# Optimization experiments

Measured on AMD Instinct MI355X. Metric: run time of the kernel, lower is better.

Reference implementation:

```python
import jax, jax.numpy as jnp
import numpy as np

N_NODES = 100000
D_IN = 256
D_OUT = 128
N_EDGES = 1600000


def setup_inputs() -> dict:
    key = jax.random.key(0)
    k1, k2, k3, k4 = jax.random.split(key, 4)
    x = jax.random.normal(k1, (N_NODES, D_IN), dtype=jnp.float32)
    edge_index = jax.random.randint(k2, (2, N_EDGES), 0, N_NODES, dtype=jnp.int64)
    # GCNConv parameters (glorot-style scale)
    W = jax.random.normal(k3, (D_IN, D_OUT), dtype=jnp.float32) * (1.0 / np.sqrt(D_IN))
    b = jax.random.normal(k4, (D_OUT,), dtype=jnp.float32) * 0.01
    return {"x": x, "edge_index": edge_index, "W": W, "b": b}


def reference(x, edge_index, W, b):
    n = x.shape[0]
    # add self-loops (PyG GCNConv default)
    loop = jnp.arange(n, dtype=edge_index.dtype)
    src = jnp.concatenate([edge_index[0], loop])
    dst = jnp.concatenate([edge_index[1], loop])
    # symmetric normalization: deg^-1/2[src] * deg^-1/2[dst]
    ones = jnp.ones(src.shape[0], dtype=x.dtype)
    deg = jax.ops.segment_sum(ones, dst, num_segments=n)
    dinv = jnp.where(deg > 0, jax.lax.rsqrt(deg), 0.0)
    norm = dinv[src] * dinv[dst]  # [E+N]
    # linear transform at nodes, then gather-scale-scatter over edges
    h = x @ W  # [N, d_out]
    msg = h[src] * norm[:, None]  # [E+N, d_out]
    out = jax.ops.segment_sum(msg, dst, num_segments=n) + b
    # CRD.forward: relu then dropout (identity in eval mode)
    return jax.nn.relu(out)
```

## Files before the change

kernel.cpp:

```cpp
#include <hip/hip_runtime.h>
#include <stdint.h>

#define D_IN 256
#define D_OUT 128
#define MAXB 800
#define NCHUNK 256

typedef __attribute__((ext_vector_type(8))) short bf16x8;
typedef __attribute__((ext_vector_type(4))) float f32x4;

__device__ __forceinline__ unsigned short f2bf(float f) {
  union { float f; uint32_t u; } v; v.f = f;
  uint32_t u = v.u;
  uint32_t r = (u + 0x7FFFu + ((u >> 16) & 1u)) >> 16;
  return (unsigned short)r;
}
__device__ __forceinline__ float bf_lo(uint32_t u) {
  union { uint32_t u; float f; } v; v.u = u << 16; return v.f;
}
__device__ __forceinline__ float bf_hi(uint32_t u) {
  union { uint32_t u; float f; } v; v.u = u & 0xFFFF0000u; return v.f;
}

__global__ __launch_bounds__(256) void k_conv_w(const float* __restrict__ W,
                                                unsigned short* __restrict__ wt) {
  int idx = blockIdx.x * 256 + threadIdx.x;
  int n = idx >> 8;
  int k = idx & 255;
  wt[idx] = f2bf(W[k * D_OUT + n]);
}

__global__ __launch_bounds__(256) void k_gemm(const float* __restrict__ x,
                                              const unsigned short* __restrict__ wt,
                                              unsigned short* __restrict__ hp, int N) {
  int wave = threadIdx.x >> 6;
  int lane = threadIdx.x & 63;
  int m = lane & 15;
  int q = lane >> 4;
  int r0 = blockIdx.x * 64 + wave * 16;
  if (r0 >= N) return;

  bf16x8 a[8];
  const float* xrow = x + (size_t)(r0 + m) * D_IN + q * 8;
#pragma unroll
  for (int kt = 0; kt < 8; ++kt) {
    float4 u0 = *reinterpret_cast<const float4*>(xrow + kt * 32);
    float4 u1 = *reinterpret_cast<const float4*>(xrow + kt * 32 + 4);
    bf16x8 av;
    av[0] = (short)f2bf(u0.x); av[1] = (short)f2bf(u0.y);
    av[2] = (short)f2bf(u0.z); av[3] = (short)f2bf(u0.w);
    av[4] = (short)f2bf(u1.x); av[5] = (short)f2bf(u1.y);
    av[6] = (short)f2bf(u1.z); av[7] = (short)f2bf(u1.w);
    a[kt] = av;
  }

#pragma unroll
  for (int nt = 0; nt < 8; ++nt) {
    f32x4 acc = {0.f, 0.f, 0.f, 0.f};
    const unsigned short* wrow = wt + (size_t)(nt * 16 + m) * D_IN + q * 8;
#pragma unroll
    for (int kt = 0; kt < 8; ++kt) {
      bf16x8 bv = *reinterpret_cast<const bf16x8*>(wrow + kt * 32);
      acc = __builtin_amdgcn_mfma_f32_16x16x32_bf16(a[kt], bv, acc, 0, 0, 0);
    }
#pragma unroll
    for (int r = 0; r < 4; ++r) {
      int row = r0 + q * 4 + r;
      hp[(size_t)row * D_OUT + nt * 16 + m] = f2bf(acc[r]);
    }
  }
}

__global__ __launch_bounds__(256) void k_passA(const int* __restrict__ ei, int E, int CH,
                                               int NB, int* __restrict__ cntm) {
  __shared__ int bins[MAXB];
  int c = blockIdx.x;
  for (int b = threadIdx.x; b < NB; b += 256) bins[b] = 0;
  __syncthreads();
  int start = c * CH, end = min(E, start + CH);
  for (int eb = start + (int)threadIdx.x * 4; eb < end; eb += 1024) {
    int kmax = end - eb; if (kmax > 4) kmax = 4;
    if (kmax == 4) {
      int4 v = *reinterpret_cast<const int4*>(ei + E + eb);
      atomicAdd(&bins[v.x >> 7], 1);
      atomicAdd(&bins[v.y >> 7], 1);
      atomicAdd(&bins[v.z >> 7], 1);
      atomicAdd(&bins[v.w >> 7], 1);
    } else {
      for (int k = 0; k < kmax; ++k) atomicAdd(&bins[ei[E + eb + k] >> 7], 1);
    }
  }
  __syncthreads();
  for (int b = threadIdx.x; b < NB; b += 256) cntm[(size_t)b * NCHUNK + c] = bins[b];
}

__global__ __launch_bounds__(NCHUNK) void k_scanB1(const int* __restrict__ cntm,
                                                   int* __restrict__ ofs,
                                                   int* __restrict__ tot) {
  __shared__ int sc[NCHUNK];
  int b = blockIdx.x, t = threadIdx.x;
  int v = cntm[(size_t)b * NCHUNK + t];
  sc[t] = v;
  __syncthreads();
  for (int off = 1; off < NCHUNK; off <<= 1) {
    int val = (t >= off) ? sc[t - off] : 0;
    __syncthreads();
    sc[t] += val;
    __syncthreads();
  }
  ofs[(size_t)b * NCHUNK + t] = sc[t] - v;
  if (t == NCHUNK - 1) tot[b] = sc[t];
}

__global__ __launch_bounds__(256) void k_scanB2(const int* __restrict__ tot,
                                                int* __restrict__ base, int NB,
                                                int* __restrict__ nptr, int N, int E) {
  __shared__ int sc[256];
  int t = threadIdx.x;
  int v[4];
  int s = 0;
#pragma unroll
  for (int j = 0; j < 4; ++j) {
    int i = t * 4 + j;
    v[j] = (i < NB) ? tot[i] : 0;
    s += v[j];
  }
  sc[t] = s;
  __syncthreads();
  for (int off = 1; off < 256; off <<= 1) {
    int val = (t >= off) ? sc[t - off] : 0;
    __syncthreads();
    sc[t] += val;
    __syncthreads();
  }
  int ex = sc[t] - s;
#pragma unroll
  for (int j = 0; j < 4; ++j) {
    int i = t * 4 + j;
    if (i < NB) base[i] = ex;
    ex += v[j];
  }
  if (t == 0) nptr[N] = E;
}

__global__ __launch_bounds__(256) void k_passC(const int* __restrict__ ei, int E, int CH,
                                               int NB, const int* __restrict__ ofs,
                                               const int* __restrict__ base,
                                               int* __restrict__ P) {
  __shared__ int cur[MAXB];
  int c = blockIdx.x;
  for (int b = threadIdx.x; b < NB; b += 256)
    cur[b] = base[b] + ofs[(size_t)b * NCHUNK + c];
  __syncthreads();
  int start = c * CH, end = min(E, start + CH);
  for (int eb = start + (int)threadIdx.x * 4; eb < end; eb += 1024) {
    int kmax = end - eb; if (kmax > 4) kmax = 4;
    int s4[4], d4[4];
    if (kmax == 4) {
      int4 vs = *reinterpret_cast<const int4*>(ei + eb);
      int4 vd = *reinterpret_cast<const int4*>(ei + E + eb);
      s4[0] = vs.x; s4[1] = vs.y; s4[2] = vs.z; s4[3] = vs.w;
      d4[0] = vd.x; d4[1] = vd.y; d4[2] = vd.z; d4[3] = vd.w;
    } else {
      for (int k = 0; k < kmax; ++k) { s4[k] = ei[eb + k]; d4[k] = ei[E + eb + k]; }
    }
#pragma unroll
    for (int k = 0; k < 4; ++k) {
      if (k >= kmax) break;
      int d = d4[k];
      int p = atomicAdd(&cur[d >> 7], 1);
      P[p] = s4[k] | ((d & 127) << 17);
    }
  }
}

__global__ __launch_bounds__(256) void k_sortd(const int* __restrict__ P,
                                               const int* __restrict__ base,
                                               const int* __restrict__ tot,
                                               int* __restrict__ nptr,
                                               float* __restrict__ dinv,
                                               int* __restrict__ P2, int N) {
  __shared__ int ideg[128];
  __shared__ int sc[128];
  __shared__ int cur[128];
  int b = blockIdx.x, t = threadIdx.x;
  if (t < 128) ideg[t] = 0;
  __syncthreads();
  int s0 = base[b], T = tot[b];
  for (int i = s0 + t; i < s0 + T; i += 256) atomicAdd(&ideg[P[i] >> 17], 1);
  __syncthreads();
  if (t < 128) sc[t] = ideg[t];
  __syncthreads();
  for (int off = 1; off < 128; off <<= 1) {
    int v = (t < 128 && t >= off) ? sc[t - off] : 0;
    __syncthreads();
    if (t < 128) sc[t] += v;
    __syncthreads();
  }
  if (t < 128) {
    int exc = s0 + sc[t] - ideg[t];
    int node = b * 128 + t;
    if (node < N) {
      nptr[node] = exc;
      dinv[node] = rsqrtf(1.0f + (float)ideg[t]);
    }
    cur[t] = exc;
  }
  __syncthreads();
  for (int i = s0 + t; i < s0 + T; i += 256) {
    int pk = P[i];
    int p = atomicAdd(&cur[pk >> 17], 1);
    P2[p] = pk & 0x1FFFF;
  }
}

__global__ __launch_bounds__(256) void k_agg(const int* __restrict__ P2,
                                             const int* __restrict__ nptr,
                                             const uint4* __restrict__ hrows,
                                             const float* __restrict__ dinv,
                                             const float* __restrict__ bias,
                                             float* __restrict__ out, int N) {
  int wave = threadIdx.x >> 6, lane = threadIdx.x & 63;
  int node = blockIdx.x * 4 + wave;
  if (node >= N) return;
  int rs = nptr[node], re = nptr[node + 1];
  int j = lane >> 4, c = lane & 15;

  float acc[8];
#pragma unroll
  for (int k = 0; k < 8; ++k) acc[k] = 0.f;

  for (int e = rs + j; e < re; e += 4) {
    int src = P2[e];
    float r = dinv[src];
    uint4 u = hrows[(size_t)src * 16 + c];
    acc[0] += r * bf_lo(u.x); acc[1] += r * bf_hi(u.x);
    acc[2] += r * bf_lo(u.y); acc[3] += r * bf_hi(u.y);
    acc[4] += r * bf_lo(u.z); acc[5] += r * bf_hi(u.z);
    acc[6] += r * bf_lo(u.w); acc[7] += r * bf_hi(u.w);
  }
#pragma unroll
  for (int k = 0; k < 8; ++k) {
    acc[k] += __shfl_xor(acc[k], 16);
    acc[k] += __shfl_xor(acc[k], 32);
  }
  if (j == 0) {
    float rsn = dinv[node];
    uint4 uh = hrows[(size_t)node * 16 + c];
    float self[8] = {bf_lo(uh.x), bf_hi(uh.x), bf_lo(uh.y), bf_hi(uh.y),
                     bf_lo(uh.z), bf_hi(uh.z), bf_lo(uh.w), bf_hi(uh.w)};
    const float4* b4 = reinterpret_cast<const float4*>(bias);
    float4 b0 = b4[c * 2], b1 = b4[c * 2 + 1];
    float bb[8] = {b0.x, b0.y, b0.z, b0.w, b1.x, b1.y, b1.z, b1.w};
    float o[8];
#pragma unroll
    for (int k = 0; k < 8; ++k) {
      float v = rsn * (acc[k] + rsn * self[k]) + bb[k];
      o[k] = v > 0.f ? v : 0.f;
    }
    float4* orow = reinterpret_cast<float4*>(out + (size_t)node * D_OUT + c * 8);
    orow[0] = float4{o[0], o[1], o[2], o[3]};
    orow[1] = float4{o[4], o[5], o[6], o[7]};
  }
}

extern "C" void kernel_launch(void* const* d_in, const int* in_sizes, int n_in,
                              void* d_out, int out_size, void* d_ws, size_t ws_size,
                              hipStream_t stream) {
  const float* x = (const float*)d_in[0];
  const int* ei = (const int*)d_in[1];
  const float* W = (const float*)d_in[2];
  const float* bias = (const float*)d_in[3];
  int N = in_sizes[0] / D_IN;
  int E = in_sizes[1] / 2;
  float* out = (float*)d_out;

  int NB = (N + 127) >> 7;
  int CH = ((E + NCHUNK - 1) / NCHUNK + 3) & ~3;

  char* w = (char*)d_ws;
  size_t off = 0;
  auto alloc = [&](size_t bytes) -> void* {
    void* p = w + off;
    off = (off + bytes + 255) & ~(size_t)255;
    return p;
  };
  unsigned short* wt = (unsigned short*)alloc((size_t)D_IN * D_OUT * 2);
  unsigned short* hp = (unsigned short*)alloc((size_t)N * D_OUT * 2);
  float* dinv = (float*)alloc((size_t)N * 4);
  int* cntm = (int*)alloc((size_t)NB * NCHUNK * 4);
  int* ofs = (int*)alloc((size_t)NB * NCHUNK * 4);
  int* tot = (int*)alloc((size_t)NB * 4);
  int* base = (int*)alloc((size_t)NB * 4);
  int* nptr = (int*)alloc((size_t)(N + 1) * 4);
  int* P = (int*)alloc((size_t)E * 4);
  int* P2 = (int*)alloc((size_t)E * 4);
  (void)ws_size; (void)n_in; (void)out_size;

  k_conv_w<<<(D_IN * D_OUT) / 256, 256, 0, stream>>>(W, wt);
  k_gemm<<<(N + 63) / 64, 256, 0, stream>>>(x, wt, hp, N);
  k_passA<<<NCHUNK, 256, 0, stream>>>(ei, E, CH, NB, cntm);
  k_scanB1<<<NB, NCHUNK, 0, stream>>>(cntm, ofs, tot);
  k_scanB2<<<1, 256, 0, stream>>>(tot, base, NB, nptr, N, E);
  k_passC<<<NCHUNK, 256, 0, stream>>>(ei, E, CH, NB, ofs, base, P);
  k_sortd<<<NB, 256, 0, stream>>>(P, base, tot, nptr, dinv, P2, N);
  k_agg<<<(N + 3) / 4, 256, 0, stream>>>(P2, nptr, (const uint4*)hp, dinv, bias, out, N);
}
```

Baseline: 326.2 us.

## Stage bf16 weights in LDS and make GEMM kernel persistent over row tiles

The GEMM kernel now copies the full transposed bf16 weight matrix (128x256, padded rows) into shared memory once per block. It also becomes a grid-stride persistent kernel with 512-thread blocks, capped at 512 blocks. Each wave then reads its B fragments from LDS instead of global/L2 on every 16-row tile, cutting repeated weight traffic. The cost is about 66KB of LDS per block, which may limit occupancy, plus a startup copy per block.

New measurement: 402.9 us. +23.5%, slower.

```diff
diff --git a/kernel.cpp b/kernel.cpp
--- a/kernel.cpp
+++ b/kernel.cpp
@@ -30,43 +30,58 @@
   wt[idx] = f2bf(W[k * D_OUT + n]);
 }
 
-__global__ __launch_bounds__(256) void k_gemm(const float* __restrict__ x,
-                                              const unsigned short* __restrict__ wt,
-                                              unsigned short* __restrict__ hp, int N) {
+#define WLP 264
+__global__ __launch_bounds__(512, 4) void k_gemm(const float* __restrict__ x,
+                                                 const unsigned short* __restrict__ wt,
+                                                 unsigned short* __restrict__ hp, int N) {
+  __shared__ unsigned short wl[128][WLP];
+
+  for (int it = threadIdx.x; it < 128 * 32; it += 512) {
+    int n = it >> 5, c = it & 31;
+    *reinterpret_cast<bf16x8*>(&wl[n][c * 8]) =
+        *reinterpret_cast<const bf16x8*>(wt + n * D_IN + c * 8);
+  }
+  __syncthreads();
+
   int wave = threadIdx.x >> 6;
   int lane = threadIdx.x & 63;
   int m = lane & 15;
   int q = lane >> 4;
-  int r0 = blockIdx.x * 64 + wave * 16;
-  if (r0 >= N) return;
-
-  bf16x8 a[8];
-  const float* xrow = x + (size_t)(r0 + m) * D_IN + q * 8;
-#pragma unroll
-  for (int kt = 0; kt < 8; ++kt) {
-    float4 u0 = *reinterpret_cast<const float4*>(xrow + kt * 32);
-    float4 u1 = *reinterpret_cast<const float4*>(xrow + kt * 32 + 4);
-    bf16x8 av;
-    av[0] = (short)f2bf(u0.x); av[1] = (short)f2bf(u0.y);
-    av[2] = (short)f2bf(u0.z); av[3] = (short)f2bf(u0.w);
-    av[4] = (short)f2bf(u1.x); av[5] = (short)f2bf(u1.y);
-    av[6] = (short)f2bf(u1.z); av[7] = (short)f2bf(u1.w);
-    a[kt] = av;
-  }
-
-#pragma unroll
-  for (int nt = 0; nt < 8; ++nt) {
-    f32x4 acc = {0.f, 0.f, 0.f, 0.f};
-    const unsigned short* wrow = wt + (size_t)(nt * 16 + m) * D_IN + q * 8;
+  int tiles = (N + 15) >> 4;
+
+  for (int t = blockIdx.x * 8 + wave; t < tiles; t += gridDim.x * 8) {
+    int r0 = t * 16;
+
+    bf16x8 a[8];
+    const float* xrow = x + (size_t)(r0 + m) * D_IN + q * 8;
 #pragma unroll
     for (int kt = 0; kt < 8; ++kt) {
-      bf16x8 bv = *reinterpret_cast<const bf16x8*>(wrow + kt * 32);
-      acc = __builtin_amdgcn_mfma_f32_16x16x32_bf16(a[kt], bv, acc, 0, 0, 0);
-    }
-#pragma unroll
-    for (int r = 0; r < 4; ++r) {
-      int row = r0 + q * 4 + r;
-      hp[(size_t)row * D_OUT + nt * 16 + m] = f2bf(acc[r]);
+      float4 u0 = *reinterpret_cast<const float4*>(xrow + kt * 32);
+      float4 u1 = *reinterpret_cast<const float4*>(xrow + kt * 32 + 4);
+      bf16x8 av;
+      av[0] = (short)f2bf(u0.x); av[1] = (short)f2bf(u0.y);
+      av[2] = (short)f2bf(u0.z); av[3] = (short)f2bf(u0.w);
+      av[4] = (short)f2bf(u1.x); av[5] = (short)f2bf(u1.y);
+      av[6] = (short)f2bf(u1.z); av[7] = (short)f2bf(u1.w);
+      a[kt] = av;
+    }
+
+#pragma unroll
+    for (int nt = 0; nt < 8; ++nt) {
+      const unsigned short* wr = &wl[nt * 16 + m][q * 8];
+      bf16x8 bv[8];
+#pragma unroll
+      for (int kt = 0; kt < 8; ++kt)
+        bv[kt] = *reinterpret_cast<const bf16x8*>(wr + kt * 32);
+      f32x4 acc = {0.f, 0.f, 0.f, 0.f};
+#pragma unroll
+      for (int kt = 0; kt < 8; ++kt)
+        acc = __builtin_amdgcn_mfma_f32_16x16x32_bf16(a[kt], bv[kt], acc, 0, 0, 0);
+#pragma unroll
+      for (int r = 0; r < 4; ++r) {
+        int row = r0 + q * 4 + r;
+        hp[(size_t)row * D_OUT + nt * 16 + m] = f2bf(acc[r]);
+      }
     }
   }
 }
@@ -297,8 +312,12 @@
   int* P2 = (int*)alloc((size_t)E * 4);
   (void)ws_size; (void)n_in; (void)out_size;
 
+  int tiles = (N + 15) >> 4;
+  int gblocks = (tiles + 7) / 8;
+  if (gblocks > 512) gblocks = 512;
+
   k_conv_w<<<(D_IN * D_OUT) / 256, 256, 0, stream>>>(W, wt);
-  k_gemm<<<(N + 63) / 64, 256, 0, stream>>>(x, wt, hp, N);
+  k_gemm<<<gblocks, 512, 0, stream>>>(x, wt, hp, N);
   k_passA<<<NCHUNK, 256, 0, stream>>>(ei, E, CH, NB, cntm);
   k_scanB1<<<NB, NCHUNK, 0, stream>>>(cntm, ofs, tot);
   k_scanB2<<<1, 256, 0, stream>>>(tot, base, NB, nptr, N, E);
```
